# Kernel tuning notes

Hardware: AMD Instinct MI355X
Metric: run time of the kernel (lower is better)

Reference implementation:

```python
import jax, jax.numpy as jnp
import numpy as np

B, C, H, W = 16, 256, 128, 128
C4, COUT = C // 4, 256


def setup_inputs() -> dict:
    key = jax.random.key(0)
    ks = jax.random.split(key, 8)
    s = 0.05
    flow = jax.random.normal(ks[0], (B, C, H, W), jnp.float32)
    de_out = jax.random.normal(ks[1], (B, C, H, W), jnp.float32)
    Wq = jax.random.normal(ks[2], (C4, C), jnp.float32) * s
    bq = jax.random.normal(ks[3], (C4,), jnp.float32) * s
    Wk = jax.random.normal(ks[4], (C4, C), jnp.float32) * s
    bk = jax.random.normal(ks[5], (C4,), jnp.float32) * s
    Wv = jax.random.normal(ks[6], (COUT, C), jnp.float32) * s
    bv = jax.random.normal(ks[7], (COUT,), jnp.float32) * s
    return {"flow": flow, "de_out": de_out, "Wq": Wq, "bq": bq,
            "Wk": Wk, "bk": bk, "Wv": Wv, "bv": bv}


def reference(flow, de_out, Wq, bq, Wk, bk, Wv, bv):
    # 1x1 convs == per-pixel channel matmuls
    q = jnp.einsum('bchw,dc->bdhw', de_out, Wq) + bq[None, :, None, None]  # [B,C4,H,W]
    k = jnp.einsum('bchw,dc->bdhw', flow, Wk) + bk[None, :, None, None]    # [B,C4,H,W]
    v = jnp.einsum('bchw,dc->bdhw', flow, Wv) + bv[None, :, None, None]    # [B,COUT,H,W]
    # height-axis attention per (batch, width) column
    energy = jnp.einsum('bdhw,bdgw->bwhg', q, k)          # [B,W,H,H], g = key height
    att = jax.nn.softmax(energy, axis=-1)                  # softmax over key height
    out = jnp.einsum('bcgw,bwhg->bchw', v, att)            # [B,COUT,H,W]
    return out
```

## Files before the change

### kernel.cpp

```cpp
#include <hip/hip_runtime.h>
#include <cstdint>
#include <cstddef>

typedef unsigned short u16;
using half4 = __attribute__((ext_vector_type(4))) _Float16;
using half8 = __attribute__((ext_vector_type(8))) _Float16;
using f32x4 = __attribute__((ext_vector_type(4))) float;
using f4    = __attribute__((ext_vector_type(4))) float;

#define B_    16
#define C_    256
#define H_    128
#define W_    128
#define C4_   64
#define COUT_ 256
#define HW_   (H_ * W_)

#define T_S       72
#define QK_S      72
#define P_S       136
#define XP_S      140
#define O_S       72

#define Q_ELEMS   ((size_t)B_ * W_ * H_ * C4_)
#define V_ELEMS   ((size_t)B_ * W_ * H_ * COUT_)
#define W16_ELEMS ((size_t)(C4_ * C_ + C4_ * C_ + COUT_ * C_))
#define WS_NEED   ((2 * Q_ELEMS + 2 * V_ELEMS + W16_ELEMS) * 2)

__device__ __forceinline__ u16 f16_rn(float f) {
  _Float16 h = (_Float16)f;
  return __builtin_bit_cast(u16, h);
}

__device__ __forceinline__ void gload16(const void* g, void* l) {
  __builtin_amdgcn_global_load_lds(
      (const __attribute__((address_space(1))) void*)g,
      (__attribute__((address_space(3))) void*)l, 16, 0, 0);
}

__global__ void __launch_bounds__(256) wconv_kernel(
    const float* __restrict__ Wk, const float* __restrict__ Wq,
    const float* __restrict__ Wv, u16* __restrict__ W16) {
  const int bid = blockIdx.x;
  const int t   = threadIdx.x;
  const float* src;
  u16* dst;
  int idx;
  if (bid < 16)      { src = Wk; dst = W16;                 idx = bid * 1024 + t * 4; }
  else if (bid < 32) { src = Wq; dst = W16 + C4_ * C_;      idx = (bid - 16) * 1024 + t * 4; }
  else               { src = Wv; dst = W16 + 2 * C4_ * C_;  idx = (bid - 32) * 1024 + t * 4; }
  f4 v = *reinterpret_cast<const f4*>(src + idx);
  half4 h;
#pragma unroll
  for (int i = 0; i < 4; ++i) h[i] = (_Float16)v[i];
  *reinterpret_cast<half4*>(dst + idx) = h;
}

__device__ __forceinline__ const half8* afragq(const u16* __restrict__ T,
                                               int w16, int ksl, int lg) {
  int oct = (ksl * 4 + lg) ^ ((w16 >> 2) & 7);
  return reinterpret_cast<const half8*>(&T[w16 * T_S + oct * 8]);
}

__device__ __forceinline__ const half8* whfrag(const u16* __restrict__ Wm16,
                                               int row, int ks, int lg) {
  return reinterpret_cast<const half8*>(Wm16 + (size_t)row * C_ + ks * 32 + lg * 8);
}

__global__ void __launch_bounds__(256, 3) qkv_kernel(
    const float* __restrict__ flow, const float* __restrict__ de_out,
    const u16* __restrict__ W16,
    const float* __restrict__ bq, const float* __restrict__ bk,
    const float* __restrict__ bv,
    u16* __restrict__ Qws, u16* __restrict__ Kws, u16* __restrict__ Vws) {
  __shared__ __align__(16) unsigned char ldsraw[2 * 16384 + 64 * T_S * 2];
  float* Fbuf[2] = {reinterpret_cast<float*>(ldsraw),
                    reinterpret_cast<float*>(ldsraw + 16384)};
  u16* T = reinterpret_cast<u16*>(ldsraw + 32768);
  u16* O = reinterpret_cast<u16*>(ldsraw);

  const int t    = threadIdx.x;
  const int bid  = blockIdx.x;
  const int g      = (bid & 7) | ((bid >> 6) << 3);
  const int hlow   = (bid >> 3) & 7;
  const int w0     = (g & 1) * 64;
  const int hgrp   = (g >> 1) & 15;
  const int b      = (g >> 5) & 15;
  const int srcsel = g >> 9;
  const int h      = hgrp * 8 + hlow;
  const int lane = t & 63;
  const int wv   = t >> 6;
  const int col  = lane & 15;
  const int lg   = lane >> 4;

  const u16* Wk16 = W16;
  const u16* Wq16 = W16 + C4_ * C_;
  const u16* Wv16 = W16 + 2 * C4_ * C_;

  const float* src =
      (srcsel ? de_out : flow) + (size_t)b * C_ * HW_ + (size_t)h * W_ + w0;

  f32x4 zero = {0.f, 0.f, 0.f, 0.f};
  f32x4 acc0[4];
  f32x4 accV[4][4];
#pragma unroll
  for (int i = 0; i < 4; ++i) acc0[i] = zero;
#pragma unroll
  for (int j = 0; j < 4; ++j)
#pragma unroll
    for (int i = 0; i < 4; ++i) accV[j][i] = zero;

#pragma unroll
  for (int i = 0; i < 4; ++i) {
    const int rr0 = wv * 16 + i * 4;
    gload16(src + (size_t)(rr0 + (lane >> 4)) * HW_ + (lane & 15) * 4,
            Fbuf[0] + rr0 * 64);
  }

#pragma unroll
  for (int q = 0; q < 4; ++q) {
    float* Fc = Fbuf[q & 1];
    float* Fn = Fbuf[(q + 1) & 1];
    if (q < 3) {
      const float* s = src + (size_t)((q + 1) * 64) * HW_;
#pragma unroll
      for (int i = 0; i < 4; ++i) {
        const int rr0 = wv * 16 + i * 4;
        gload16(s + (size_t)(rr0 + (lane >> 4)) * HW_ + (lane & 15) * 4,
                Fn + rr0 * 64);
      }
      asm volatile("s_waitcnt vmcnt(4) lgkmcnt(0)\ns_barrier" ::: "memory");
    } else {
      asm volatile("s_waitcnt vmcnt(0) lgkmcnt(0)\ns_barrier" ::: "memory");
    }
    __builtin_amdgcn_sched_barrier(0);

#pragma unroll
    for (int i = 0; i < 2; ++i) {
      const int flat = i * 256 + t;
      const int wq = flat & 15;
      const int pp = flat >> 4;
      const f4 fa = *reinterpret_cast<const f4*>(&Fc[(2 * pp) * 64 + wq * 4]);
      const f4 fb = *reinterpret_cast<const f4*>(&Fc[(2 * pp + 1) * 64 + wq * 4]);
      const int c_loc = 2 * pp;
      const int oct   = (c_loc >> 3) ^ (wq & 7);
#pragma unroll
      for (int j = 0; j < 4; ++j) {
        const int w = wq * 4 + j;
        uint32_t pk = (uint32_t)f16_rn(fa[j]) | ((uint32_t)f16_rn(fb[j]) << 16);
        *reinterpret_cast<uint32_t*>(&T[w * T_S + oct * 8 + (c_loc & 7)]) = pk;
      }
    }
    asm volatile("s_waitcnt lgkmcnt(0)\ns_barrier" ::: "memory");
    __builtin_amdgcn_sched_barrier(0);

#pragma unroll
    for (int ksl = 0; ksl < 2; ++ksl) {
      const int ks = 2 * q + ksl;
      if (srcsel == 0) {
        const half8 bK = *whfrag(Wk16, wv * 16 + col, ks, lg);
        half8 bV[4];
#pragma unroll
        for (int j = 0; j < 4; ++j)
          bV[j] = *whfrag(Wv16, (wv * 4 + j) * 16 + col, ks, lg);
#pragma unroll
        for (int wt = 0; wt < 4; ++wt) {
          const half8 afr = *afragq(T, wt * 16 + col, ksl, lg);
          acc0[wt] = __builtin_amdgcn_mfma_f32_16x16x32_f16(afr, bK, acc0[wt], 0, 0, 0);
#pragma unroll
          for (int j = 0; j < 4; ++j)
            accV[j][wt] =
                __builtin_amdgcn_mfma_f32_16x16x32_f16(afr, bV[j], accV[j][wt], 0, 0, 0);
        }
      } else {
        const half8 bQ = *whfrag(Wq16, wv * 16 + col, ks, lg);
#pragma unroll
        for (int wt = 0; wt < 4; ++wt) {
          const half8 afr = *afragq(T, wt * 16 + col, ksl, lg);
          acc0[wt] = __builtin_amdgcn_mfma_f32_16x16x32_f16(afr, bQ, acc0[wt], 0, 0, 0);
        }
      }
    }
  }

  if (srcsel == 0) {
    {
      const float bias = bk[wv * 16 + col];
      __syncthreads();
#pragma unroll
      for (int wt = 0; wt < 4; ++wt)
#pragma unroll
        for (int r = 0; r < 4; ++r)
          O[(wt * 16 + lg * 4 + r) * O_S + wv * 16 + col] = f16_rn(acc0[wt][r] + bias);
      __syncthreads();
#pragma unroll
      for (int i = 0; i < 2; ++i) {
        const int item = i * 256 + t;
        const int wl = item >> 3;
        const int d0 = (item & 7) * 8;
        *reinterpret_cast<half8*>(
            &Kws[(((size_t)b * W_ + w0 + wl) * H_ + h) * C4_ + d0]) =
            *reinterpret_cast<const half8*>(&O[wl * O_S + d0]);
      }
    }
#pragma unroll
    for (int j = 0; j < 4; ++j) {
      const int co = (wv * 4 + j) * 16 + col;
      const float bias = bv[co];
#pragma unroll
      for (int wt = 0; wt < 4; ++wt)
#pragma unroll
        for (int r = 0; r < 4; ++r) {
          int w = w0 + wt * 16 + lg * 4 + r;
          Vws[(size_t)(b * W_ + w) * 32768 + ((h >> 3) * COUT_ + co) * 8 + (h & 7)] =
              f16_rn(accV[j][wt][r] + bias);
        }
    }
  } else {
    const float bias = bq[wv * 16 + col];
    __syncthreads();
#pragma unroll
    for (int wt = 0; wt < 4; ++wt)
#pragma unroll
      for (int r = 0; r < 4; ++r)
        O[(wt * 16 + lg * 4 + r) * O_S + wv * 16 + col] = f16_rn(acc0[wt][r] + bias);
    __syncthreads();
#pragma unroll
    for (int i = 0; i < 2; ++i) {
      const int item = i * 256 + t;
      const int wl = item >> 3;
      const int d0 = (item & 7) * 8;
      *reinterpret_cast<half8*>(
          &Qws[(((size_t)b * W_ + w0 + wl) * H_ + h) * C4_ + d0]) =
          *reinterpret_cast<const half8*>(&O[wl * O_S + d0]);
    }
  }
}

template <int EPI>
__global__ void __launch_bounds__(256) attn_kernel(
    const u16* __restrict__ Qws, const u16* __restrict__ Kws,
    const u16* __restrict__ Vws, u16* __restrict__ out_tmp,
    float* __restrict__ out) {
  __shared__ __align__(16) u16 ldsQK[2 * 128 * QK_S];

  const int t   = threadIdx.x;
  const int bid = blockIdx.x;
  const int sw  = (bid & 7) * 256 + (bid >> 3);
  const int b   = sw >> 7;
  const int w   = sw & 127;
  const int lane = t & 63;
  const int wv   = t >> 6;
  const int col  = lane & 15;
  const int lg   = lane >> 4;

  const u16* qc    = Qws + ((size_t)b * W_ + w) * H_ * C4_;
  const u16* kc    = Kws + ((size_t)b * W_ + w) * H_ * C4_;
  const u16* vbase = Vws + (size_t)(b * W_ + w) * 32768;

  u16* ldsQ = ldsQK;
  u16* ldsK = ldsQK + 128 * QK_S;

#pragma unroll
  for (int i = 0; i < 4; ++i) {
    int item = i * 256 + t;
    int hh   = item >> 3;
    int d0   = (item & 7) * 8;
    *reinterpret_cast<half8*>(&ldsQ[hh * QK_S + d0]) =
        *reinterpret_cast<const half8*>(qc + item * 8);
    *reinterpret_cast<half8*>(&ldsK[hh * QK_S + d0]) =
        *reinterpret_cast<const half8*>(kc + item * 8);
  }
  __syncthreads();

  f32x4 zero = {0.f, 0.f, 0.f, 0.f};
  f32x4 e[2][8];
#pragma unroll
  for (int ht = 0; ht < 2; ++ht)
#pragma unroll
    for (int gt = 0; gt < 8; ++gt) e[ht][gt] = zero;

#pragma unroll
  for (int ks = 0; ks < 2; ++ks) {
    half8 aq[2];
#pragma unroll
    for (int ht = 0; ht < 2; ++ht)
      aq[ht] = *reinterpret_cast<const half8*>(
          &ldsQ[(wv * 32 + ht * 16 + col) * QK_S + ks * 32 + lg * 8]);
#pragma unroll
    for (int gt = 0; gt < 8; ++gt) {
      const half8 bk_ = *reinterpret_cast<const half8*>(
          &ldsK[(gt * 16 + col) * QK_S + ks * 32 + lg * 8]);
#pragma unroll
      for (int ht = 0; ht < 2; ++ht)
        e[ht][gt] = __builtin_amdgcn_mfma_f32_16x16x32_f16(aq[ht], bk_, e[ht][gt], 0, 0, 0);
    }
  }
  __syncthreads();

  u16* ldsP = ldsQK + wv * 32 * P_S;

#pragma unroll
  for (int ht = 0; ht < 2; ++ht)
#pragma unroll
    for (int r = 0; r < 4; ++r) {
      float m = -1e30f;
#pragma unroll
      for (int gt = 0; gt < 8; ++gt) m = fmaxf(m, e[ht][gt][r]);
#pragma unroll
      for (int off = 1; off < 16; off <<= 1) m = fmaxf(m, __shfl_xor(m, off));
      float s = 0.f;
#pragma unroll
      for (int gt = 0; gt < 8; ++gt) {
        float p = __expf(e[ht][gt][r] - m);
        e[ht][gt][r] = p;
        s += p;
      }
#pragma unroll
      for (int off = 1; off < 16; off <<= 1) s += __shfl_xor(s, off);
      const float inv = 1.f / s;
      const int hh = ht * 16 + lg * 4 + r;
#pragma unroll
      for (int gt = 0; gt < 8; ++gt)
        ldsP[hh * P_S + gt * 16 + col] = f16_rn(e[ht][gt][r] * inv);
    }

  f32x4 o[2][16];
#pragma unroll
  for (int ht = 0; ht < 2; ++ht)
#pragma unroll
    for (int ct = 0; ct < 16; ++ct) o[ht][ct] = zero;

#pragma unroll
  for (int ks = 0; ks < 4; ++ks) {
    half8 ap[2];
#pragma unroll
    for (int ht = 0; ht < 2; ++ht)
      ap[ht] = *reinterpret_cast<const half8*>(
          &ldsP[(ht * 16 + col) * P_S + ks * 32 + lg * 8]);
#pragma unroll
    for (int ct = 0; ct < 16; ++ct) {
      const half8 bv_ = *reinterpret_cast<const half8*>(
          vbase + ((ks * 4 + lg) * COUT_ + ct * 16 + col) * 8);
#pragma unroll
      for (int ht = 0; ht < 2; ++ht)
        o[ht][ct] = __builtin_amdgcn_mfma_f32_16x16x32_f16(ap[ht], bv_, o[ht][ct], 0, 0, 0);
    }
  }

  if (EPI == 1) {
    u16* ldsX = ldsQK;
    u16* dst_col = out_tmp + ((size_t)(b * W_ + w) << 15);
#pragma unroll
    for (int ctg = 0; ctg < 4; ++ctg) {
      __syncthreads();
#pragma unroll
      for (int j = 0; j < 4; ++j) {
        const int ct    = ctg * 4 + j;
        const int c_loc = j * 16 + col;
#pragma unroll
        for (int ht = 0; ht < 2; ++ht) {
          const int hbase = wv * 32 + ht * 16 + lg * 4;
          half4 pk;
#pragma unroll
          for (int r = 0; r < 4; ++r) pk[r] = (_Float16)o[ht][ct][r];
          *reinterpret_cast<half4*>(&ldsX[c_loc * XP_S + hbase]) = pk;
        }
      }
      __syncthreads();
      const int c_loc = t >> 2;
      const int h0    = (t & 3) * 32;
      u16* dp = dst_col + (ctg * 64 + c_loc) * 128 + h0;
#pragma unroll
      for (int k = 0; k < 4; ++k)
        *reinterpret_cast<half8*>(dp + k * 8) =
            *reinterpret_cast<const half8*>(&ldsX[c_loc * XP_S + h0 + k * 8]);
    }
  } else {
    float* outp = out + (size_t)b * COUT_ * HW_ + w;
#pragma unroll
    for (int ht = 0; ht < 2; ++ht)
#pragma unroll
      for (int ct = 0; ct < 16; ++ct)
#pragma unroll
        for (int r = 0; r < 4; ++r) {
          int hrow = wv * 32 + ht * 16 + lg * 4 + r;
          int c = ct * 16 + col;
          outp[((size_t)c * H_ + hrow) * W_] = o[ht][ct][r];
        }
  }
}

__global__ void __launch_bounds__(256) transpose_kernel(
    const u16* __restrict__ T, float* __restrict__ out) {
  __shared__ float lds[64 * 132];
  const int t   = threadIdx.x;
  const int bid = blockIdx.x;
  const int b   = bid >> 9;
  const int ft  = bid & 511;

  {
    const int w  = t >> 1;
    const int fo = (t & 1) * 32;
    const u16* src = T + ((size_t)(b * W_ + w) << 15) + ft * 64 + fo;
#pragma unroll
    for (int k = 0; k < 4; ++k) {
      half8 v = *reinterpret_cast<const half8*>(src + k * 8);
#pragma unroll
      for (int e = 0; e < 8; ++e)
        lds[(fo + k * 8 + e) * 132 + w] = (float)v[e];
    }
  }
  __syncthreads();
  {
    const int f_loc = t >> 2;
    const int w0    = (t & 3) * 32;
    float* dst = out + (size_t)b * (COUT_ * HW_) + (size_t)(ft * 64 + f_loc) * 128 + w0;
#pragma unroll
    for (int k = 0; k < 8; ++k) {
      f4 v4;
#pragma unroll
      for (int e = 0; e < 4; ++e) v4[e] = lds[f_loc * 132 + w0 + k * 4 + e];
      *reinterpret_cast<f4*>(dst + k * 4) = v4;
    }
  }
}

extern "C" void kernel_launch(void* const* d_in, const int* in_sizes, int n_in,
                              void* d_out, int out_size, void* d_ws, size_t ws_size,
                              hipStream_t stream) {
  const float* flow   = (const float*)d_in[0];
  const float* de_out = (const float*)d_in[1];
  const float* Wq = (const float*)d_in[2];
  const float* bq = (const float*)d_in[3];
  const float* Wk = (const float*)d_in[4];
  const float* bk = (const float*)d_in[5];
  const float* Wv = (const float*)d_in[6];
  const float* bv = (const float*)d_in[7];
  float* out = (float*)d_out;

  u16* Qws = (u16*)d_ws;
  u16* Kws = Qws + Q_ELEMS;
  u16* Vws = Kws + Q_ELEMS;
  u16* W16 = Vws + V_ELEMS;
  u16* Tws = W16 + W16_ELEMS;

  wconv_kernel<<<96, 256, 0, stream>>>(Wk, Wq, Wv, W16);
  qkv_kernel<<<2 * B_ * H_ * 2, 256, 0, stream>>>(flow, de_out, W16, bq, bk, bv,
                                                  Qws, Kws, Vws);
  if (ws_size >= (size_t)WS_NEED) {
    attn_kernel<1><<<B_ * W_, 256, 0, stream>>>(Qws, Kws, Vws, Tws, out);
    transpose_kernel<<<B_ * 512, 256, 0, stream>>>(Tws, out);
  } else {
    attn_kernel<0><<<B_ * W_, 256, 0, stream>>>(Qws, Kws, Vws, Tws, out);
  }
}
```

Before: 539.1 us.

## Retile QKV projection blocks to 8x8 pixel tiles for vectorized V stores

Each QKV projection block now covers an 8-wide by 8-tall pixel tile instead of a 64-wide row segment at one height. With this shape each lane's accumulator rows map to 4 consecutive heights, so V can be written as half4 vector stores into the h-octet packed layout instead of scattered 2-byte stores. Global loads become 32-byte row segments across 8 rows, which are less contiguous than the previous 256-byte rows and may reduce load efficiency. The LDS transpose indexing and swizzle are updated to match.

Measured after the change: 550.3 us. 2.1% more time.

```diff
diff --git a/kernel.cpp b/kernel.cpp
--- a/kernel.cpp
+++ b/kernel.cpp
@@ -57,9 +57,9 @@
 }
 
 __device__ __forceinline__ const half8* afragq(const u16* __restrict__ T,
-                                               int w16, int ksl, int lg) {
-  int oct = (ksl * 4 + lg) ^ ((w16 >> 2) & 7);
-  return reinterpret_cast<const half8*>(&T[w16 * T_S + oct * 8]);
+                                               int prow, int ksl, int lg) {
+  int oct = (ksl * 4 + lg) ^ ((prow >> 2) & 7);
+  return reinterpret_cast<const half8*>(&T[prow * T_S + oct * 8]);
 }
 
 __device__ __forceinline__ const half8* whfrag(const u16* __restrict__ Wm16,
@@ -81,13 +81,13 @@
 
   const int t    = threadIdx.x;
   const int bid  = blockIdx.x;
-  const int g      = (bid & 7) | ((bid >> 6) << 3);
-  const int hlow   = (bid >> 3) & 7;
-  const int w0     = (g & 1) * 64;
-  const int hgrp   = (g >> 1) & 15;
-  const int b      = (g >> 5) & 15;
-  const int srcsel = g >> 9;
-  const int h      = hgrp * 8 + hlow;
+  const int xcd    = bid & 7;
+  const int wtlow  = (bid >> 3) & 1;
+  const int ggg    = bid >> 4;
+  const int wt     = xcd * 2 + wtlow;
+  const int h8     = ggg & 15;
+  const int b      = (ggg >> 4) & 15;
+  const int srcsel = ggg >> 8;
   const int lane = t & 63;
   const int wv   = t >> 6;
   const int col  = lane & 15;
@@ -97,8 +97,8 @@
   const u16* Wq16 = W16 + C4_ * C_;
   const u16* Wv16 = W16 + 2 * C4_ * C_;
 
-  const float* src =
-      (srcsel ? de_out : flow) + (size_t)b * C_ * HW_ + (size_t)h * W_ + w0;
+  const float* src = (srcsel ? de_out : flow) +
+                     (size_t)b * C_ * HW_ + (size_t)(h8 * 8) * W_ + wt * 8;
 
   f32x4 zero = {0.f, 0.f, 0.f, 0.f};
   f32x4 acc0[4];
@@ -110,25 +110,24 @@
 #pragma unroll
     for (int i = 0; i < 4; ++i) accV[j][i] = zero;
 
-#pragma unroll
-  for (int i = 0; i < 4; ++i) {
-    const int rr0 = wv * 16 + i * 4;
-    gload16(src + (size_t)(rr0 + (lane >> 4)) * HW_ + (lane & 15) * 4,
-            Fbuf[0] + rr0 * 64);
-  }
+#define ISSUE_QTR(FDST, CBASE)                                               \
+  {                                                                          \
+    _Pragma("unroll") for (int i = 0; i < 4; ++i) {                          \
+      const int rr0 = wv * 16 + i * 4;                                       \
+      gload16(src + (size_t)((CBASE) + rr0 + (lane >> 4)) * HW_ +            \
+                  ((lane >> 1) & 7) * W_ + (lane & 1) * 4,                   \
+              (FDST) + rr0 * 64);                                            \
+    }                                                                        \
+  }
+
+  ISSUE_QTR(Fbuf[0], 0)
 
 #pragma unroll
   for (int q = 0; q < 4; ++q) {
     float* Fc = Fbuf[q & 1];
     float* Fn = Fbuf[(q + 1) & 1];
     if (q < 3) {
-      const float* s = src + (size_t)((q + 1) * 64) * HW_;
-#pragma unroll
-      for (int i = 0; i < 4; ++i) {
-        const int rr0 = wv * 16 + i * 4;
-        gload16(s + (size_t)(rr0 + (lane >> 4)) * HW_ + (lane & 15) * 4,
-                Fn + rr0 * 64);
-      }
+      ISSUE_QTR(Fn, (q + 1) * 64)
       asm volatile("s_waitcnt vmcnt(4) lgkmcnt(0)\ns_barrier" ::: "memory");
     } else {
       asm volatile("s_waitcnt vmcnt(0) lgkmcnt(0)\ns_barrier" ::: "memory");
@@ -138,17 +137,19 @@
 #pragma unroll
     for (int i = 0; i < 2; ++i) {
       const int flat = i * 256 + t;
-      const int wq = flat & 15;
-      const int pp = flat >> 4;
-      const f4 fa = *reinterpret_cast<const f4*>(&Fc[(2 * pp) * 64 + wq * 4]);
-      const f4 fb = *reinterpret_cast<const f4*>(&Fc[(2 * pp + 1) * 64 + wq * 4]);
-      const int c_loc = 2 * pp;
-      const int oct   = (c_loc >> 3) ^ (wq & 7);
+      const int cp = flat >> 4;
+      const int hl = (flat >> 1) & 7;
+      const int wq = flat & 1;
+      const f4 fa = *reinterpret_cast<const f4*>(&Fc[(2 * cp) * 64 + hl * 8 + wq * 4]);
+      const f4 fb = *reinterpret_cast<const f4*>(&Fc[(2 * cp + 1) * 64 + hl * 8 + wq * 4]);
+      const int c_loc = 2 * cp;
 #pragma unroll
       for (int j = 0; j < 4; ++j) {
         const int w = wq * 4 + j;
+        const int p = w * 8 + hl;
+        const int oct = (cp >> 2) ^ ((p >> 2) & 7);
         uint32_t pk = (uint32_t)f16_rn(fa[j]) | ((uint32_t)f16_rn(fb[j]) << 16);
-        *reinterpret_cast<uint32_t*>(&T[w * T_S + oct * 8 + (c_loc & 7)]) = pk;
+        *reinterpret_cast<uint32_t*>(&T[p * T_S + oct * 8 + (c_loc & 7)]) = pk;
       }
     }
     asm volatile("s_waitcnt lgkmcnt(0)\ns_barrier" ::: "memory");
@@ -164,20 +165,20 @@
         for (int j = 0; j < 4; ++j)
           bV[j] = *whfrag(Wv16, (wv * 4 + j) * 16 + col, ks, lg);
 #pragma unroll
-        for (int wt = 0; wt < 4; ++wt) {
-          const half8 afr = *afragq(T, wt * 16 + col, ksl, lg);
-          acc0[wt] = __builtin_amdgcn_mfma_f32_16x16x32_f16(afr, bK, acc0[wt], 0, 0, 0);
+        for (int mt = 0; mt < 4; ++mt) {
+          const half8 afr = *afragq(T, mt * 16 + col, ksl, lg);
+          acc0[mt] = __builtin_amdgcn_mfma_f32_16x16x32_f16(afr, bK, acc0[mt], 0, 0, 0);
 #pragma unroll
           for (int j = 0; j < 4; ++j)
-            accV[j][wt] =
-                __builtin_amdgcn_mfma_f32_16x16x32_f16(afr, bV[j], accV[j][wt], 0, 0, 0);
+            accV[j][mt] =
+                __builtin_amdgcn_mfma_f32_16x16x32_f16(afr, bV[j], accV[j][mt], 0, 0, 0);
         }
       } else {
         const half8 bQ = *whfrag(Wq16, wv * 16 + col, ks, lg);
 #pragma unroll
-        for (int wt = 0; wt < 4; ++wt) {
-          const half8 afr = *afragq(T, wt * 16 + col, ksl, lg);
-          acc0[wt] = __builtin_amdgcn_mfma_f32_16x16x32_f16(afr, bQ, acc0[wt], 0, 0, 0);
+        for (int mt = 0; mt < 4; ++mt) {
+          const half8 afr = *afragq(T, mt * 16 + col, ksl, lg);
+          acc0[mt] = __builtin_amdgcn_mfma_f32_16x16x32_f16(afr, bQ, acc0[mt], 0, 0, 0);
         }
       }
     }
@@ -188,53 +189,59 @@
       const float bias = bk[wv * 16 + col];
       __syncthreads();
 #pragma unroll
-      for (int wt = 0; wt < 4; ++wt)
+      for (int mt = 0; mt < 4; ++mt)
 #pragma unroll
         for (int r = 0; r < 4; ++r)
-          O[(wt * 16 + lg * 4 + r) * O_S + wv * 16 + col] = f16_rn(acc0[wt][r] + bias);
+          O[(mt * 16 + lg * 4 + r) * O_S + wv * 16 + col] = f16_rn(acc0[mt][r] + bias);
       __syncthreads();
 #pragma unroll
       for (int i = 0; i < 2; ++i) {
         const int item = i * 256 + t;
-        const int wl = item >> 3;
+        const int p  = item >> 3;
         const int d0 = (item & 7) * 8;
         *reinterpret_cast<half8*>(
-            &Kws[(((size_t)b * W_ + w0 + wl) * H_ + h) * C4_ + d0]) =
-            *reinterpret_cast<const half8*>(&O[wl * O_S + d0]);
-      }
-    }
-#pragma unroll
-    for (int j = 0; j < 4; ++j) {
-      const int co = (wv * 4 + j) * 16 + col;
-      const float bias = bv[co];
-#pragma unroll
-      for (int wt = 0; wt < 4; ++wt)
-#pragma unroll
-        for (int r = 0; r < 4; ++r) {
-          int w = w0 + wt * 16 + lg * 4 + r;
-          Vws[(size_t)(b * W_ + w) * 32768 + ((h >> 3) * COUT_ + co) * 8 + (h & 7)] =
-              f16_rn(accV[j][wt][r] + bias);
+            &Kws[(((size_t)b * W_ + wt * 8 + (p >> 3)) * H_ + h8 * 8 + (p & 7)) * C4_ + d0]) =
+            *reinterpret_cast<const half8*>(&O[p * O_S + d0]);
+      }
+    }
+    {
+      const size_t colbase = ((size_t)b * W_ + wt * 8) * 32768;
+#pragma unroll
+      for (int j = 0; j < 4; ++j) {
+        const int co = (wv * 4 + j) * 16 + col;
+        const float bias = bv[co];
+#pragma unroll
+        for (int mt = 0; mt < 4; ++mt) {
+          const int w_loc = mt * 2 + (lg >> 1);
+          const int hl0   = (lg & 1) * 4;
+          half4 pk;
+#pragma unroll
+          for (int r = 0; r < 4; ++r) pk[r] = (_Float16)(accV[j][mt][r] + bias);
+          *reinterpret_cast<half4*>(
+              Vws + colbase + (size_t)w_loc * 32768 + (size_t)(h8 * COUT_ + co) * 8 + hl0) = pk;
         }
+      }
     }
   } else {
     const float bias = bq[wv * 16 + col];
     __syncthreads();
 #pragma unroll
-    for (int wt = 0; wt < 4; ++wt)
+    for (int mt = 0; mt < 4; ++mt)
 #pragma unroll
       for (int r = 0; r < 4; ++r)
-        O[(wt * 16 + lg * 4 + r) * O_S + wv * 16 + col] = f16_rn(acc0[wt][r] + bias);
+        O[(mt * 16 + lg * 4 + r) * O_S + wv * 16 + col] = f16_rn(acc0[mt][r] + bias);
     __syncthreads();
 #pragma unroll
     for (int i = 0; i < 2; ++i) {
       const int item = i * 256 + t;
-      const int wl = item >> 3;
+      const int p  = item >> 3;
       const int d0 = (item & 7) * 8;
       *reinterpret_cast<half8*>(
-          &Qws[(((size_t)b * W_ + w0 + wl) * H_ + h) * C4_ + d0]) =
-          *reinterpret_cast<const half8*>(&O[wl * O_S + d0]);
-    }
-  }
+          &Qws[(((size_t)b * W_ + wt * 8 + (p >> 3)) * H_ + h8 * 8 + (p & 7)) * C4_ + d0]) =
+          *reinterpret_cast<const half8*>(&O[p * O_S + d0]);
+    }
+  }
+#undef ISSUE_QTR
 }
 
 template <int EPI>
```
